# Optimization experiments

Hardware: AMD Instinct MI355X
Metric: run time of the kernel (lower is better)

Reference implementation:

```python
import jax, jax.numpy as jnp
import numpy as np

B, C, H, W = 32, 3, 512, 512
EPS = 1e-8


def _radius_bins(h, w):
    cy, cx = h // 2, w // 2
    y = jnp.arange(h, dtype=jnp.float32) - cy
    x = jnp.arange(w, dtype=jnp.float32) - cx
    radius = jnp.sqrt(y[:, None] ** 2 + x[None, :] ** 2)  # [H, W]
    max_r = min(cy, cx)
    bins = jnp.floor(radius).astype(jnp.int32)
    # pixels with radius >= max_r fall outside all bins in the original loop;
    # route them to a dummy overflow bin that we drop afterwards.
    bins = jnp.where(bins < max_r, bins, max_r)
    return bins.reshape(-1), max_r


def _psd(x):
    f = jnp.fft.fft2(x)                  # over last two dims, like torch.fft.fft2
    psd = jnp.abs(f) ** 2
    return jnp.log(psd + EPS)            # log_power=True


def _radial_average(psd):
    b, c, h, w = psd.shape
    bins, max_r = _radius_bins(h, w)     # [H*W], static
    data = psd.reshape(b * c, h * w).T   # [H*W, B*C]
    sums = jax.ops.segment_sum(data, bins, num_segments=max_r + 1)
    counts = jax.ops.segment_sum(jnp.ones((h * w,), psd.dtype), bins,
                                 num_segments=max_r + 1)
    avg = jnp.where(counts[:, None] > 0, sums / counts[:, None], 0.0)
    avg = avg[:max_r]                    # drop overflow bin -> [max_r, B*C]
    return avg.T.reshape(b, c, max_r)


def setup_inputs() -> dict:
    key = jax.random.key(0)
    k1, k2 = jax.random.split(key)
    predicted = jax.random.normal(k1, (B, C, H, W), dtype=jnp.float32)
    target = jax.random.normal(k2, (B, C, H, W), dtype=jnp.float32)
    return {"predicted": predicted, "target": target}


def reference(predicted, target):
    pred_rad = _radial_average(_psd(predicted))
    targ_rad = _radial_average(_psd(target))
    return jnp.mean(jnp.abs(pred_rad - targ_rad))  # l1, reduction='mean'
```

## Files before the change

### kernel.cpp

```cpp
#include <hip/hip_runtime.h>
#include <math.h>

#define HH 512
#define WW 512
#define IMG (HH*WW)
#define NIMG_PER 96
#define NIMG 192
#define NBIN 256
#define EPSV 1e-8f

#define CSTR 264
#define IMGC (512*CSTR)
#define NTILE 33
#define SLOT 580

__device__ __forceinline__ int drev(int s) {
    return ((s & 7) << 6) | (s & 56) | (s >> 6);
}
__device__ __forceinline__ int fsw(int a) { return a + (a >> 3); }

__device__ __forceinline__ float2 cmul(float2 a, float2 b) {
    return make_float2(a.x*b.x - a.y*b.y, a.x*b.y + a.y*b.x);
}
#define C_ADD(a,b) make_float2((a).x+(b).x, (a).y+(b).y)
#define C_SUB(a,b) make_float2((a).x-(b).x, (a).y-(b).y)
#define C_NI(a)    make_float2((a).y, -(a).x)

__device__ __forceinline__ void bfly8(float2 x[8]) {
    const float R = 0.70710678118654752440f;
    float2 t0=C_ADD(x[0],x[4]), t4=C_SUB(x[0],x[4]);
    float2 t1=C_ADD(x[1],x[5]), t5=C_SUB(x[1],x[5]);
    float2 t2=C_ADD(x[2],x[6]), t6=C_SUB(x[2],x[6]);
    float2 t3=C_ADD(x[3],x[7]), t7=C_SUB(x[3],x[7]);
    float2 u0=C_ADD(t0,t2), u2=C_SUB(t0,t2);
    float2 u1=C_ADD(t1,t3), u3=C_SUB(t1,t3);
    x[0]=C_ADD(u0,u1); x[4]=C_SUB(u0,u1);
    { float2 n3 = C_NI(u3); x[2]=C_ADD(u2,n3); x[6]=C_SUB(u2,n3); }
    float2 s1 = make_float2(R*(t5.x + t5.y), R*(t5.y - t5.x));
    float2 s2 = C_NI(t6);
    float2 s3 = make_float2(R*(t7.y - t7.x), -R*(t7.x + t7.y));
    float2 v0=C_ADD(t4,s2), v2=C_SUB(t4,s2);
    float2 v1=C_ADD(s1,s3), v3=C_SUB(s1,s3);
    x[1]=C_ADD(v0,v1); x[5]=C_SUB(v0,v1);
    { float2 n3 = C_NI(v3); x[3]=C_ADD(v2,n3); x[7]=C_SUB(v2,n3); }
}

__device__ __forceinline__ void twiddle7(float2* x, float ang) {
    const float sn = __sinf(ang), cs = __cosf(ang);
    const float2 w1 = make_float2(cs, sn);
    const float2 w2 = cmul(w1, w1);
    const float2 w3 = cmul(w2, w1);
    const float2 w4 = cmul(w2, w2);
    const float2 w5 = cmul(w2, w3);
    const float2 w6 = cmul(w3, w3);
    const float2 w7 = cmul(w3, w4);
    x[1]=cmul(x[1],w1); x[2]=cmul(x[2],w2); x[3]=cmul(x[3],w3);
    x[4]=cmul(x[4],w4); x[5]=cmul(x[5],w5); x[6]=cmul(x[6],w6);
    x[7]=cmul(x[7],w7);
}

__global__ __launch_bounds__(256) void rowfft_kernel(
    const float* __restrict__ pred, const float* __restrict__ targ,
    float2* __restrict__ out, int img_base)
{
    __shared__ float2 sd[2320];
    const int t = threadIdx.x;

    const int pb = blockIdx.x;
    const int li = blockIdx.y;
    const int g  = img_base + li;
    const float* img = (g < NIMG_PER) ? (pred + (size_t)g * IMG)
                                      : (targ + (size_t)(g - NIMG_PER) * IMG);
    const float4* src4 = (const float4*)(img + (size_t)(pb*8) * WW);

    #pragma unroll
    for (int it = 0; it < 2; ++it) {
        const int id = it*256 + t;
        const int s  = id >> 7;
        const int x4 = id & 127;
        const float4 va = src4[(2*s)   * 128 + x4];
        const float4 vb = src4[(2*s+1) * 128 + x4];
        float2* p = sd + s*SLOT + (4*x4 + (x4 >> 1));
        p[0] = make_float2(va.x, vb.x);
        p[1] = make_float2(va.y, vb.y);
        p[2] = make_float2(va.z, vb.z);
        p[3] = make_float2(va.w, vb.w);
    }
    __syncthreads();

    const int i = t & 63;
    float2* p = sd + (t >> 6) * SLOT;
    float2 x[8];

    #pragma unroll
    for (int j = 0; j < 8; ++j) x[j] = p[fsw(i + 64*j)];
    bfly8(x);
    twiddle7(x, -0.012271846303085130f * (float)i);
    #pragma unroll
    for (int j = 0; j < 8; ++j) p[fsw(i + 64*j)] = x[j];
    __syncthreads();

    const int grp = i >> 3, i2 = i & 7;
    #pragma unroll
    for (int j = 0; j < 8; ++j) x[j] = p[fsw(64*grp + i2 + 8*j)];
    bfly8(x);
    twiddle7(x, -0.098174770424681038f * (float)i2);
    #pragma unroll
    for (int j = 0; j < 8; ++j) p[fsw(64*grp + i2 + 8*j)] = x[j];
    __syncthreads();

    #pragma unroll
    for (int j = 0; j < 8; ++j) x[j] = p[fsw(8*i + j)];
    bfly8(x);
    #pragma unroll
    for (int j = 0; j < 8; ++j) p[fsw(8*i + j)] = x[j];
    __syncthreads();

    const int w_ = t >> 6;
    const int k  = (w_ > 0) ? (((t & 7) << 6) | (t & 56) | w_)
                            : ((t < 32) ? (8*t + 4) : (8*(t - 32)));
    const int kk = (k <= 256) ? k : (512 - k);
    const int a1 = fsw(drev(kk));
    const int a2 = fsw(drev((512 - kk) & 511));
    const int a3 = fsw(drev(256));

    float2 A[4], Bv[4], Z[4];
    #pragma unroll
    for (int s = 0; s < 4; ++s) {
        const float2 P = sd[s*SLOT + a1];
        const float2 Q = sd[s*SLOT + a2];
        A[s]  = make_float2(0.5f*(P.x + Q.x), 0.5f*(P.y - Q.y));
        Bv[s] = make_float2(0.5f*(P.y + Q.y), 0.5f*(Q.x - P.x));
        Z[s]  = sd[s*SLOT + a3];
    }
    __syncthreads();

    {
        const int fb = fsw(kk);
        #pragma unroll
        for (int s = 0; s < 4; ++s) {
            sd[(2*s+0)*290 + fb] = A[s];
            sd[(2*s+1)*290 + fb] = Bv[s];
        }
    }
    if (t == 0) {
        const int fb = fsw(256);
        #pragma unroll
        for (int s = 0; s < 4; ++s) {
            sd[(2*s+0)*290 + fb] = make_float2(Z[s].x, 0.0f);
            sd[(2*s+1)*290 + fb] = make_float2(Z[s].y, 0.0f);
        }
    }
    __syncthreads();

    float2* dst = out + (size_t)li * IMGC + (size_t)(pb*8) * CSTR;
    #pragma unroll
    for (int r = 0; r < 8; ++r) {
        dst[(size_t)r * CSTR + t] = sd[r*290 + fsw(t)];
        if (t < 8) {
            float2 v = make_float2(0.0f, 0.0f);
            if (t == 0) v = sd[r*290 + fsw(256)];
            dst[(size_t)r * CSTR + 256 + t] = v;
        }
    }
}

__global__ __launch_bounds__(256) void colfft_kernel(
    const float2* __restrict__ in, float* __restrict__ bins2, int img_base)
{
    __shared__ float2 sd[8*SLOT];
    __shared__ float  bs[4*257];
    const int t = threadIdx.x;
    for (int id = t; id < 4*257; id += 256) bs[id] = 0.0f;

    const int li = blockIdx.y;
    const int x0 = blockIdx.x * 8;
    const float2* src = in + (size_t)li * IMGC;

    #pragma unroll
    for (int it = 0; it < 16; ++it) {
        const int id = it*256 + t;
        const int y  = id >> 3;
        const int cl = id & 7;
        sd[cl*SLOT + fsw(y)] = src[(size_t)y * CSTR + (x0 + cl)];
    }
    __syncthreads();

    const int i  = t & 63;
    const int c0 = t >> 6;
    float2 x[2][8];

    #pragma unroll
    for (int sl = 0; sl < 2; ++sl) {
        float2* p = sd + (c0 + 4*sl)*SLOT;
        #pragma unroll
        for (int j = 0; j < 8; ++j) x[sl][j] = p[fsw(i + 64*j)];
        bfly8(x[sl]);
    }
    {
        const float ang = -0.012271846303085130f * (float)i;
        const float sn = __sinf(ang), cs = __cosf(ang);
        const float2 w1 = make_float2(cs, sn);
        const float2 w2 = cmul(w1,w1), w3 = cmul(w2,w1), w4 = cmul(w2,w2);
        const float2 w5 = cmul(w2,w3), w6 = cmul(w3,w3), w7 = cmul(w3,w4);
        #pragma unroll
        for (int sl = 0; sl < 2; ++sl) {
            x[sl][1]=cmul(x[sl][1],w1); x[sl][2]=cmul(x[sl][2],w2);
            x[sl][3]=cmul(x[sl][3],w3); x[sl][4]=cmul(x[sl][4],w4);
            x[sl][5]=cmul(x[sl][5],w5); x[sl][6]=cmul(x[sl][6],w6);
            x[sl][7]=cmul(x[sl][7],w7);
        }
    }
    #pragma unroll
    for (int sl = 0; sl < 2; ++sl) {
        float2* p = sd + (c0 + 4*sl)*SLOT;
        #pragma unroll
        for (int j = 0; j < 8; ++j) p[fsw(i + 64*j)] = x[sl][j];
    }
    __syncthreads();

    const int grp = i >> 3, i2 = i & 7;
    #pragma unroll
    for (int sl = 0; sl < 2; ++sl) {
        float2* p = sd + (c0 + 4*sl)*SLOT;
        #pragma unroll
        for (int j = 0; j < 8; ++j) x[sl][j] = p[fsw(64*grp + i2 + 8*j)];
        bfly8(x[sl]);
    }
    {
        const float ang = -0.098174770424681038f * (float)i2;
        const float sn = __sinf(ang), cs = __cosf(ang);
        const float2 w1 = make_float2(cs, sn);
        const float2 w2 = cmul(w1,w1), w3 = cmul(w2,w1), w4 = cmul(w2,w2);
        const float2 w5 = cmul(w2,w3), w6 = cmul(w3,w3), w7 = cmul(w3,w4);
        #pragma unroll
        for (int sl = 0; sl < 2; ++sl) {
            x[sl][1]=cmul(x[sl][1],w1); x[sl][2]=cmul(x[sl][2],w2);
            x[sl][3]=cmul(x[sl][3],w3); x[sl][4]=cmul(x[sl][4],w4);
            x[sl][5]=cmul(x[sl][5],w5); x[sl][6]=cmul(x[sl][6],w6);
            x[sl][7]=cmul(x[sl][7],w7);
        }
    }
    #pragma unroll
    for (int sl = 0; sl < 2; ++sl) {
        float2* p = sd + (c0 + 4*sl)*SLOT;
        #pragma unroll
        for (int j = 0; j < 8; ++j) p[fsw(64*grp + i2 + 8*j)] = x[sl][j];
    }
    __syncthreads();

    #pragma unroll
    for (int sl = 0; sl < 2; ++sl) {
        float2* p = sd + (c0 + 4*sl)*SLOT;
        float2 y8[8];
        #pragma unroll
        for (int j = 0; j < 8; ++j) y8[j] = p[fsw(8*i + j)];
        bfly8(y8);
        #pragma unroll
        for (int j = 0; j < 8; ++j) p[fsw(8*i + j)] = y8[j];
    }
    __syncthreads();

    {
        const int cl2 = t & 7;
        const int h   = t >> 3;
        const int kx  = x0 + cl2;
        const bool valid = (kx <= 256);
        const float scale = (kx == 0 || kx == 256) ? 0.5f : 1.0f;
        const int dxsq = (kx - 256) * (kx - 256);
        const int rep  = (t & 3) * 257;

        float acc = 0.0f;
        int prevb = 1000;
        #pragma unroll
        for (int j = 0; j < 16; ++j) {
            const int q = 64*(j & 7) + 8*((2*h + (j >> 3)) & 7) + (h >> 2);
            const float2 v = sd[cl2*SLOT + fsw(q)];
            const float val = __logf(v.x*v.x + v.y*v.y + EPSV) * scale;
            const int dy = 16*h + j - 256;
            const int b  = (int)sqrtf((float)(dy*dy + dxsq));
            if (b != prevb) {
                if (prevb < NBIN && valid) atomicAdd(&bs[rep + prevb], acc);
                prevb = b; acc = val;
            } else {
                acc += val;
            }
        }
        if (prevb < NBIN && valid) atomicAdd(&bs[rep + prevb], acc);
    }
    __syncthreads();

    const float v = 2.0f * (bs[t] + bs[257 + t] + bs[514 + t] + bs[771 + t]);
    bins2[((size_t)blockIdx.x * NIMG + (img_base + li)) * NBIN + t] = v;
}

__global__ __launch_bounds__(256) void reduce_kernel(
    const float* __restrict__ bins2, float* __restrict__ bins)
{
    const int li = blockIdx.x;
    const int t  = threadIdx.x;
    float s = 0.0f;
    #pragma unroll
    for (int tile = 0; tile < NTILE; ++tile)
        s += bins2[((size_t)tile * NIMG + li) * NBIN + t];
    bins[(size_t)li * NBIN + t] = s;
}

__global__ __launch_bounds__(256) void counts_kernel(float* __restrict__ cnt)
{
    __shared__ float c[NBIN];
    const int t = threadIdx.x;
    c[t] = 0.0f;
    __syncthreads();

    const int base = blockIdx.x * 4096;
    #pragma unroll
    for (int i = 0; i < 16; ++i) {
        const int id = base + i * 256 + t;
        const int y = id >> 9, xx = id & 511;
        const int dy = y - 256, dx = xx - 256;
        const int b  = (int)sqrtf((float)(dy*dy + dx*dx));
        if (b < NBIN) atomicAdd(&c[b], 1.0f);
    }
    __syncthreads();
    if (c[t] != 0.0f) atomicAdd(&cnt[t], c[t]);
}

__global__ __launch_bounds__(256) void finalize_kernel(
    const float* __restrict__ bins, const float* __restrict__ cnt,
    float* __restrict__ out)
{
    __shared__ float red[256];
    const int t = threadIdx.x;

    float acc = 0.0f;
    for (int id = t; id < NIMG_PER * NBIN; id += 256) {
        const int i = id >> 8;
        const int r = id & 255;
        const float d = fabsf(bins[(size_t)i * NBIN + r]
                            - bins[(size_t)(NIMG_PER + i) * NBIN + r]);
        acc += d / cnt[r];
    }
    red[t] = acc;
    __syncthreads();
    for (int w = 128; w > 0; w >>= 1) {
        if (t < w) red[t] += red[t + w];
        __syncthreads();
    }
    if (t == 0) out[0] = red[0] / (float)(NIMG_PER * NBIN);
}

extern "C" void kernel_launch(void* const* d_in, const int* in_sizes, int n_in,
                              void* d_out, int out_size, void* d_ws, size_t ws_size,
                              hipStream_t stream)
{
    const float* pred = (const float*)d_in[0];
    const float* targ = (const float*)d_in[1];
    float* out = (float*)d_out;

    char* ws = (char*)d_ws;
    float* cnt   = (float*)ws;
    float* bins  = cnt + NBIN;
    float* bins2 = bins + (size_t)NIMG * NBIN;
    const size_t fixed_f = NBIN + (size_t)NIMG*NBIN + (size_t)NTILE*NIMG*NBIN;
    const size_t off = (fixed_f*sizeof(float) + 255) & ~(size_t)255;
    float2* cbuf = (float2*)(ws + off);

    const size_t per_img = (size_t)IMGC * sizeof(float2);
    size_t avail = (ws_size > off) ? (ws_size - off) : 0;
    int chunk = (int)(avail / per_img);
    if (chunk > NIMG) chunk = NIMG;
    if (chunk < 1) chunk = 1;

    hipMemsetAsync(cnt, 0, NBIN * sizeof(float), stream);
    counts_kernel<<<dim3(64), dim3(256), 0, stream>>>(cnt);

    for (int base = 0; base < NIMG; base += chunk) {
        const int n = (NIMG - base < chunk) ? (NIMG - base) : chunk;
        dim3 gA(HH / 8, n), gB(NTILE, n), blk(256);
        rowfft_kernel<<<gA, blk, 0, stream>>>(pred, targ, cbuf, base);
        colfft_kernel<<<gB, blk, 0, stream>>>(cbuf, bins2, base);
    }

    reduce_kernel<<<dim3(NIMG), dim3(256), 0, stream>>>(bins2, bins);
    finalize_kernel<<<dim3(1), dim3(256), 0, stream>>>(bins, cnt, out);
}
```

Before: 238.7 us.

## Store row-FFT output transposed and make column FFT wave-local

The row FFT kernel now writes its half-spectrum transposed (column-major, 257 columns by 512), using float4 stores, in place of the padded row-major layout. This lets each wave of the column FFT kernel read its two columns directly from global memory into registers, dropping the shared-memory staging load and its block barrier. Later stages use wave-level barriers instead of block-wide __syncthreads, and each wave keeps its own pair of histogram bins to cut atomic contention. The cost is larger shared bins and strided per-thread column reads, which may be less coalesced.

```diff
diff --git a/kernel.cpp b/kernel.cpp
--- a/kernel.cpp
+++ b/kernel.cpp
@@ -9,8 +9,7 @@
 #define NBIN 256
 #define EPSV 1e-8f
 
-#define CSTR 264
-#define IMGC (512*CSTR)
+#define IMGC (257*512)
 #define NTILE 33
 #define SLOT 580
 
@@ -25,6 +24,12 @@
 #define C_ADD(a,b) make_float2((a).x+(b).x, (a).y+(b).y)
 #define C_SUB(a,b) make_float2((a).x-(b).x, (a).y-(b).y)
 #define C_NI(a)    make_float2((a).y, -(a).x)
+
+__device__ __forceinline__ void wsync() {
+    asm volatile("" ::: "memory");
+    __builtin_amdgcn_wave_barrier();
+    asm volatile("" ::: "memory");
+}
 
 __device__ __forceinline__ void bfly8(float2 x[8]) {
     const float R = 0.70710678118654752440f;
@@ -153,14 +158,23 @@
     }
     __syncthreads();
 
-    float2* dst = out + (size_t)li * IMGC + (size_t)(pb*8) * CSTR;
-    #pragma unroll
-    for (int r = 0; r < 8; ++r) {
-        dst[(size_t)r * CSTR + t] = sd[r*290 + fsw(t)];
-        if (t < 8) {
-            float2 v = make_float2(0.0f, 0.0f);
-            if (t == 0) v = sd[r*290 + fsw(256)];
-            dst[(size_t)r * CSTR + 256 + t] = v;
+    {
+        float2 p8[8];
+        const int fc = fsw(t);
+        #pragma unroll
+        for (int r = 0; r < 8; ++r) p8[r] = sd[r*290 + fc];
+        float4* d4 = (float4*)(out + (size_t)li * IMGC + (size_t)t * 512 + pb*8);
+        #pragma unroll
+        for (int q = 0; q < 4; ++q)
+            d4[q] = make_float4(p8[2*q].x, p8[2*q].y, p8[2*q+1].x, p8[2*q+1].y);
+        if (t == 0) {
+            const int fc2 = fsw(256);
+            #pragma unroll
+            for (int r = 0; r < 8; ++r) p8[r] = sd[r*290 + fc2];
+            float4* e4 = (float4*)(out + (size_t)li * IMGC + (size_t)256 * 512 + pb*8);
+            #pragma unroll
+            for (int q = 0; q < 4; ++q)
+                e4[q] = make_float4(p8[2*q].x, p8[2*q].y, p8[2*q+1].x, p8[2*q+1].y);
         }
     }
 }
@@ -169,32 +183,27 @@
     const float2* __restrict__ in, float* __restrict__ bins2, int img_base)
 {
     __shared__ float2 sd[8*SLOT];
-    __shared__ float  bs[4*257];
-    const int t = threadIdx.x;
-    for (int id = t; id < 4*257; id += 256) bs[id] = 0.0f;
-
-    const int li = blockIdx.y;
-    const int x0 = blockIdx.x * 8;
+    __shared__ float  bs[8*257];
+    const int t    = threadIdx.x;
+    const int lane = t & 63;
+    const int w    = t >> 6;
+
+    for (int id = lane; id < 514; id += 64) bs[w*514 + id] = 0.0f;
+
+    const int li    = blockIdx.y;
+    const int x0    = blockIdx.x * 8;
+    const int cbase = x0 + 2*w;
     const float2* src = in + (size_t)li * IMGC;
 
-    #pragma unroll
-    for (int it = 0; it < 16; ++it) {
-        const int id = it*256 + t;
-        const int y  = id >> 3;
-        const int cl = id & 7;
-        sd[cl*SLOT + fsw(y)] = src[(size_t)y * CSTR + (x0 + cl)];
-    }
-    __syncthreads();
-
-    const int i  = t & 63;
-    const int c0 = t >> 6;
+    const int i = lane;
     float2 x[2][8];
 
     #pragma unroll
     for (int sl = 0; sl < 2; ++sl) {
-        float2* p = sd + (c0 + 4*sl)*SLOT;
-        #pragma unroll
-        for (int j = 0; j < 8; ++j) x[sl][j] = p[fsw(i + 64*j)];
+        const int kx = cbase + sl;
+        const float2* col = src + (size_t)(kx <= 256 ? kx : 256) * 512;
+        #pragma unroll
+        for (int j = 0; j < 8; ++j) x[sl][j] = col[i + 64*j];
         bfly8(x[sl]);
     }
     {
@@ -211,18 +220,21 @@
             x[sl][7]=cmul(x[sl][7],w7);
         }
     }
+    {
+        float2* p0 = sd + (2*w+0)*SLOT;
+        float2* p1 = sd + (2*w+1)*SLOT;
+        #pragma unroll
+        for (int j = 0; j < 8; ++j) {
+            const int a = fsw(i + 64*j);
+            p0[a] = x[0][j]; p1[a] = x[1][j];
+        }
+    }
+    wsync();
+
+    const int grp = i >> 3, i2 = i & 7;
     #pragma unroll
     for (int sl = 0; sl < 2; ++sl) {
-        float2* p = sd + (c0 + 4*sl)*SLOT;
-        #pragma unroll
-        for (int j = 0; j < 8; ++j) p[fsw(i + 64*j)] = x[sl][j];
-    }
-    __syncthreads();
-
-    const int grp = i >> 3, i2 = i & 7;
-    #pragma unroll
-    for (int sl = 0; sl < 2; ++sl) {
-        float2* p = sd + (c0 + 4*sl)*SLOT;
+        float2* p = sd + (2*w+sl)*SLOT;
         #pragma unroll
         for (int j = 0; j < 8; ++j) x[sl][j] = p[fsw(64*grp + i2 + 8*j)];
         bfly8(x[sl]);
@@ -243,15 +255,15 @@
     }
     #pragma unroll
     for (int sl = 0; sl < 2; ++sl) {
-        float2* p = sd + (c0 + 4*sl)*SLOT;
+        float2* p = sd + (2*w+sl)*SLOT;
         #pragma unroll
         for (int j = 0; j < 8; ++j) p[fsw(64*grp + i2 + 8*j)] = x[sl][j];
     }
-    __syncthreads();
+    wsync();
 
     #pragma unroll
     for (int sl = 0; sl < 2; ++sl) {
-        float2* p = sd + (c0 + 4*sl)*SLOT;
+        float2* p = sd + (2*w+sl)*SLOT;
         float2 y8[8];
         #pragma unroll
         for (int j = 0; j < 8; ++j) y8[j] = p[fsw(8*i + j)];
@@ -259,39 +271,42 @@
         #pragma unroll
         for (int j = 0; j < 8; ++j) p[fsw(8*i + j)] = y8[j];
     }
-    __syncthreads();
-
-    {
-        const int cl2 = t & 7;
-        const int h   = t >> 3;
-        const int kx  = x0 + cl2;
+    wsync();
+
+    {
+        const int cl2 = lane & 1;
+        const int h   = lane >> 1;
+        const int kx  = cbase + cl2;
         const bool valid = (kx <= 256);
         const float scale = (kx == 0 || kx == 256) ? 0.5f : 1.0f;
         const int dxsq = (kx - 256) * (kx - 256);
-        const int rep  = (t & 3) * 257;
+        float* bsw = bs + w*514 + ((h & 1) ? 257 : 0);
+        const float2* p = sd + (2*w+cl2)*SLOT;
 
         float acc = 0.0f;
         int prevb = 1000;
         #pragma unroll
         for (int j = 0; j < 16; ++j) {
             const int q = 64*(j & 7) + 8*((2*h + (j >> 3)) & 7) + (h >> 2);
-            const float2 v = sd[cl2*SLOT + fsw(q)];
+            const float2 v = p[fsw(q)];
             const float val = __logf(v.x*v.x + v.y*v.y + EPSV) * scale;
             const int dy = 16*h + j - 256;
             const int b  = (int)sqrtf((float)(dy*dy + dxsq));
             if (b != prevb) {
-                if (prevb < NBIN && valid) atomicAdd(&bs[rep + prevb], acc);
+                if (prevb < NBIN && valid) atomicAdd(&bsw[prevb], acc);
                 prevb = b; acc = val;
             } else {
                 acc += val;
             }
         }
-        if (prevb < NBIN && valid) atomicAdd(&bs[rep + prevb], acc);
-    }
-    __syncthreads();
-
-    const float v = 2.0f * (bs[t] + bs[257 + t] + bs[514 + t] + bs[771 + t]);
-    bins2[((size_t)blockIdx.x * NIMG + (img_base + li)) * NBIN + t] = v;
+        if (prevb < NBIN && valid) atomicAdd(&bsw[prevb], acc);
+    }
+    __syncthreads();
+
+    float v = 0.0f;
+    #pragma unroll
+    for (int r = 0; r < 8; ++r) v += bs[r*257 + t];
+    bins2[((size_t)blockIdx.x * NIMG + (img_base + li)) * NBIN + t] = 2.0f * v;
 }
 
 __global__ __launch_bounds__(256) void reduce_kernel(
```

Result: slower. 267.2 us (+12.0%).
